# Kernel tuning notes

Measured on AMD Instinct MI355X. Metric: run time of the kernel, lower is better.

## Reference

```python
import jax, jax.numpy as jnp
import numpy as np

MAX_LENGTH = 10
SOS = 0
H = 1024
V = 32000
B = 256
S = 64


def setup_inputs() -> dict:
    key = jax.random.key(0)
    ks = jax.random.split(key, 16)
    sc = 1.0 / np.sqrt(H)
    return {
        "encoder_outputs": jax.random.normal(ks[0], (B, S, H), jnp.float32),
        "encoder_hidden": jax.random.normal(ks[1], (1, B, H), jnp.float32),
        "target_tensor": jax.random.randint(ks[2], (B, MAX_LENGTH), 0, V),
        "embedding": jax.random.normal(ks[3], (V, H), jnp.float32),
        "Wa_w": jax.random.uniform(ks[4], (H, H), jnp.float32, -sc, sc),
        "Wa_b": jax.random.uniform(ks[5], (H,), jnp.float32, -sc, sc),
        "Ua_w": jax.random.uniform(ks[6], (H, H), jnp.float32, -sc, sc),
        "Ua_b": jax.random.uniform(ks[7], (H,), jnp.float32, -sc, sc),
        "Va_w": jax.random.uniform(ks[8], (1, H), jnp.float32, -sc, sc),
        "Va_b": jax.random.uniform(ks[9], (1,), jnp.float32, -sc, sc),
        "gru_w_ih": jax.random.uniform(ks[10], (3 * H, 2 * H), jnp.float32, -sc, sc),
        "gru_w_hh": jax.random.uniform(ks[11], (3 * H, H), jnp.float32, -sc, sc),
        "gru_b_ih": jax.random.uniform(ks[12], (3 * H,), jnp.float32, -sc, sc),
        "gru_b_hh": jax.random.uniform(ks[13], (3 * H,), jnp.float32, -sc, sc),
        "out_w": jax.random.uniform(ks[14], (V, H), jnp.float32, -sc, sc),
        "out_b": jax.random.uniform(ks[15], (V,), jnp.float32, -sc, sc),
    }


def reference(encoder_outputs, encoder_hidden, target_tensor, embedding,
              Wa_w, Wa_b, Ua_w, Ua_b, Va_w, Va_b,
              gru_w_ih, gru_w_hh, gru_b_ih, gru_b_hh, out_w, out_b):
    keys = encoder_outputs                      # [B,S,H]
    # Ua(keys) is step-invariant: hoist out of the decode loop.
    Uk = jnp.einsum('bsh,kh->bsk', keys, Ua_w) + Ua_b  # [B,S,H]
    h0 = encoder_hidden[0]                      # [B,H]
    # teacher forcing: input at step i is SOS for i=0 else target[:, i-1]
    toks = jnp.concatenate(
        [jnp.full((B, 1), SOS, dtype=target_tensor.dtype),
         target_tensor[:, :MAX_LENGTH - 1]], axis=1).T  # [T,B]

    def step(h, tok):
        emb = embedding[tok]                               # [B,H] (dropout = identity in eval)
        wq = jnp.dot(h, Wa_w.T) + Wa_b                     # [B,H]
        e = jnp.tanh(wq[:, None, :] + Uk)                  # [B,S,H]
        scores = jnp.einsum('bsh,h->bs', e, Va_w[0]) + Va_b[0]
        w = jax.nn.softmax(scores, axis=-1)                # [B,S]
        ctx = jnp.einsum('bs,bsh->bh', w, keys)            # [B,H]
        x = jnp.concatenate([emb, ctx], axis=-1)           # [B,2H]
        gi = jnp.dot(x, gru_w_ih.T) + gru_b_ih             # [B,3H]
        gh = jnp.dot(h, gru_w_hh.T) + gru_b_hh             # [B,3H]
        ir, iz, inn = jnp.split(gi, 3, axis=-1)
        hr, hz, hn = jnp.split(gh, 3, axis=-1)
        r = jax.nn.sigmoid(ir + hr)
        z = jax.nn.sigmoid(iz + hz)
        n = jnp.tanh(inn + r * hn)
        h2 = (1.0 - z) * n + z * h                         # [B,H]
        logits = jnp.dot(h2, out_w.T) + out_b              # [B,V]
        return h2, (logits, w)

    h_last, (logits, attn) = jax.lax.scan(step, h0, toks)
    dec_out = jax.nn.log_softmax(jnp.transpose(logits, (1, 0, 2)), axis=-1)  # [B,T,V]
    attentions = jnp.transpose(attn, (1, 0, 2))            # [B,T,S]
    return dec_out, h_last[None, :, :], attentions
```

## Files before the change

kernel.cpp:

```cpp
#include <hip/hip_runtime.h>
#include <math.h>

#define H 1024
#define V 32000
#define B 256
#define S 64
#define T 10

#define GBK 32

typedef __attribute__((ext_vector_type(8))) short bf16x8;
typedef __attribute__((ext_vector_type(4))) float f32x4;

static __device__ __forceinline__ unsigned short f2bf(float f) {
  unsigned int u = __float_as_uint(f);
  u += 0x7fff + ((u >> 16) & 1);
  return (unsigned short)(u >> 16);
}
static __device__ __forceinline__ float bf2f(unsigned short u) {
  return __uint_as_float(((unsigned int)u) << 16);
}
static __device__ __forceinline__ float fast_tanh(float x) {
  float e = __expf(2.f * x);
  return 1.f - 2.f * __builtin_amdgcn_rcpf(e + 1.f);
}
static __device__ __forceinline__ float fast_sigmoid(float x) {
  return __builtin_amdgcn_rcpf(1.f + __expf(-x));
}

static __device__ __forceinline__ void load_lds16(const void* g, void* l) {
  __builtin_amdgcn_global_load_lds(
      (const __attribute__((address_space(1))) unsigned int*)g,
      (__attribute__((address_space(3))) unsigned int*)l, 16, 0, 0);
}

static __device__ __forceinline__ int lds_off(int row, int g) {
  return row * GBK + ((g ^ ((row >> 1) & 3)) * 8);
}

template <int TM, int TN, int MODE, int GRIDMODE, int STAGES>
__global__ __launch_bounds__(256) void gemm_mfma(
    const unsigned short* __restrict__ A, const unsigned short* __restrict__ W,
    const float* __restrict__ aux, float* __restrict__ C,
    int M, int N, int K, int ldc) {
  constexpr int FM = TM / 32;
  constexpr int FN = TN / 32;
  constexpr int CA = TM / 64;
  constexpr int CB = TN / 64;
  constexpr int LOADS = CA + CB;
  constexpr int F = (STAGES >= 3) ? (STAGES - 2) : 0;

  __shared__ unsigned short lsA[STAGES][TM * GBK];
  __shared__ unsigned short lsB[STAGES][TN * GBK];
  const int tid = threadIdx.x;
  const int lane = tid & 63;
  const int w = tid >> 6;

  int mIdx, nIdx;
  if constexpr (GRIDMODE == 1) {
    const int nwg = gridDim.x * gridDim.y;
    const int orig = blockIdx.y * gridDim.x + blockIdx.x;
    const int q = nwg >> 3, rr = nwg & 7;
    const int xcd = orig & 7, rest = orig >> 3;
    const int wgid =
        (xcd < rr ? xcd * (q + 1) : rr * (q + 1) + (xcd - rr) * q) + rest;
    mIdx = wgid % gridDim.x;
    nIdx = wgid / gridDim.x;
  } else {
    mIdx = blockIdx.y;
    nIdx = blockIdx.x;
  }
  const int mBase = mIdx * TM;
  const int nBase = nIdx * TN;
  const int rowBase = (w >> 1) * (TM / 2);
  const int colBase = (w & 1) * (TN / 2);

  const int fr = lane & 15;
  const int fkU = lane >> 4;
  const int fg = lane >> 4;

  f32x4 acc[FM][FN] = {};

  auto STAGE = [&](int buf, int k0) {
#pragma unroll
    for (int i = 0; i < CA; ++i) {
      int chunk = i * 256 + tid;
      int row = chunk >> 2;
      int u = chunk & 3;
      int col = (u ^ ((row >> 1) & 3)) * 8;
      load_lds16(A + (size_t)(mBase + row) * K + k0 + col,
                 &lsA[buf][chunk * 8]);
    }
#pragma unroll
    for (int i = 0; i < CB; ++i) {
      int chunk = i * 256 + tid;
      int row = chunk >> 2;
      int u = chunk & 3;
      int col = (u ^ ((row >> 1) & 3)) * 8;
      load_lds16(W + (size_t)(nBase + row) * K + k0 + col,
                 &lsB[buf][chunk * 8]);
    }
  };

  const int NT = K / GBK;
  for (int s = 0; s <= F && s < NT; ++s) STAGE(s % STAGES, s * GBK);

  for (int t = 0; t < NT; ++t) {
    const int rem = NT - 1 - t;
    if (rem >= F) {
      asm volatile("s_waitcnt vmcnt(%0)\n\ts_barrier" :: "i"(F * LOADS)
                   : "memory");
    } else if (rem == 2) {
      asm volatile("s_waitcnt vmcnt(%0)\n\ts_barrier" :: "i"(2 * LOADS)
                   : "memory");
    } else if (rem == 1) {
      asm volatile("s_waitcnt vmcnt(%0)\n\ts_barrier" :: "i"(1 * LOADS)
                   : "memory");
    } else {
      asm volatile("s_waitcnt vmcnt(0)\n\ts_barrier" ::: "memory");
    }
    if (t + F + 1 < NT) STAGE((t + F + 1) % STAGES, (t + F + 1) * GBK);

    const int cb = t % STAGES;
    bf16x8 af[FM], bfr[FN];
#pragma unroll
    for (int m = 0; m < FM; ++m)
      af[m] = *(const bf16x8*)&lsA[cb][lds_off(rowBase + m * 16 + fr, fkU)];
#pragma unroll
    for (int n = 0; n < FN; ++n)
      bfr[n] = *(const bf16x8*)&lsB[cb][lds_off(colBase + n * 16 + fr, fkU)];
#pragma unroll
    for (int m = 0; m < FM; ++m)
#pragma unroll
      for (int n = 0; n < FN; ++n)
        acc[m][n] = __builtin_amdgcn_mfma_f32_16x16x32_bf16(
            af[m], bfr[n], acc[m][n], 0, 0, 0);
  }

#pragma unroll
  for (int m = 0; m < FM; ++m) {
    int colg[FN];
    float bv[FN];
#pragma unroll
    for (int n = 0; n < FN; ++n) {
      colg[n] = nBase + colBase + n * 16 + fr;
      if constexpr (MODE != 2) bv[n] = aux[colg[n]];
    }
#pragma unroll
    for (int r = 0; r < 4; ++r) {
      const int rowg = mBase + rowBase + m * 16 + fg * 4 + r;
      float v[FN];
#pragma unroll
      for (int n = 0; n < FN; ++n) {
        if constexpr (MODE == 2)
          v[n] = acc[m][n][r] + aux[(size_t)rowg * ldc + colg[n]];
        else
          v[n] = acc[m][n][r] + bv[n];
        C[(size_t)rowg * ldc + colg[n]] = v[n];
      }
    }
  }
}

__global__ __launch_bounds__(256) void gemm_gru3(
    const unsigned short* __restrict__ A,
    const unsigned short* __restrict__ W3,
    const float* __restrict__ giE_t,
    const float* __restrict__ wqgh,
    const float* __restrict__ h_in,
    float* __restrict__ h_out,
    unsigned short* __restrict__ h_out_bf,
    unsigned char* __restrict__ h_out_f8) {
  constexpr int BK = 64;
  constexpr int STAGES = 3;
  constexpr int LOADS = 5;
  __shared__ unsigned short lsA[STAGES][64 * BK];
  __shared__ unsigned short lsW[STAGES][96 * BK];
  const int tid = threadIdx.x;
  const int lane = tid & 63;
  const int w = tid >> 6;
  const int mBase = blockIdx.x * 64;
  const int jBase = blockIdx.y * 32;
  const int fr = lane & 15;
  const int fkU = lane >> 4;
  const int fg = lane >> 4;

  f32x4 acc[6] = {};

  auto STAGE = [&](int buf, int k0) {
#pragma unroll
    for (int i = 0; i < 2; ++i) {
      int c = i * 256 + tid;
      int row = c >> 3, u = c & 7;
      int col = (u ^ (row & 7)) * 8;
      load_lds16(A + (size_t)(mBase + row) * H + k0 + col, &lsA[buf][c * 8]);
    }
#pragma unroll
    for (int i = 0; i < 3; ++i) {
      int c = i * 256 + tid;
      int wr = c >> 3, u = c & 7;
      int gate = wr >> 5, jj = wr & 31;
      int col = (u ^ (wr & 7)) * 8;
      load_lds16(W3 + (size_t)(gate * H + jBase + jj) * H + k0 + col,
                 &lsW[buf][c * 8]);
    }
  };

  const int NT = H / BK;
  STAGE(0, 0);
  STAGE(1, BK);
  for (int t = 0; t < NT; ++t) {
    const int rem = NT - 1 - t;
    if (rem >= 1) {
      asm volatile("s_waitcnt vmcnt(%0)\n\ts_barrier" :: "i"(LOADS)
                   : "memory");
    } else {
      asm volatile("s_waitcnt vmcnt(0)\n\ts_barrier" ::: "memory");
    }
    if (t + 2 < NT) STAGE((t + 2) % STAGES, (t + 2) * BK);
    const int cb = t % STAGES;
    const int arow = w * 16 + fr;
#pragma unroll
    for (int ks = 0; ks < 2; ++ks) {
      const int u = ks * 4 + fkU;
      bf16x8 af =
          *(const bf16x8*)&lsA[cb][arow * BK + ((u ^ (arow & 7)) * 8)];
#pragma unroll
      for (int n = 0; n < 6; ++n) {
        int wr = n * 16 + fr;
        bf16x8 bf =
            *(const bf16x8*)&lsW[cb][wr * BK + ((u ^ (wr & 7)) * 8)];
        acc[n] = __builtin_amdgcn_mfma_f32_16x16x32_bf16(af, bf, acc[n],
                                                         0, 0, 0);
      }
    }
  }

#pragma unroll
  for (int r = 0; r < 4; ++r) {
    const int b = mBase + w * 16 + fg * 4 + r;
    const float* giE_row = giE_t + (size_t)b * 3 * H;
    const float* gh_row = wqgh + (size_t)b * 4 * H + H;
#pragma unroll
    for (int jjg = 0; jjg < 2; ++jjg) {
      const int col = jBase + jjg * 16 + fr;
      float gr = acc[0 + jjg][r] + giE_row[col];
      float gz = acc[2 + jjg][r] + giE_row[H + col];
      float gn = acc[4 + jjg][r] + giE_row[2 * H + col];
      float rr = fast_sigmoid(gr + gh_row[col]);
      float zz = fast_sigmoid(gz + gh_row[H + col]);
      float nn = fast_tanh(gn + rr * gh_row[2 * H + col]);
      float hp = h_in[(size_t)b * H + col];
      float ho = (1.f - zz) * nn + zz * hp;
      h_out[(size_t)b * H + col] = ho;
      h_out_bf[(size_t)b * H + col] = f2bf(ho);
      int p8 = __builtin_amdgcn_cvt_pk_fp8_f32(ho, ho, 0, false);
      h_out_f8[(size_t)b * H + col] = (unsigned char)(p8 & 0xff);
    }
  }
}

template <int MODE>
__global__ __launch_bounds__(256) void gemm_fp8(
    const unsigned char* __restrict__ A8, const unsigned char* __restrict__ W8,
    const float* __restrict__ bias, unsigned short* __restrict__ Cb,
    unsigned char* __restrict__ C8, float* __restrict__ partials,
    int M, int N, int K, int ldc, int pstride) {
  constexpr int BK = 64;
  __shared__ __align__(16) unsigned char lsA[2][128 * BK];
  __shared__ __align__(16) unsigned char lsB[2][128 * BK];
  const int tid = threadIdx.x;
  const int lane = tid & 63;
  const int w = tid >> 6;

  const int nwg = gridDim.x * gridDim.y;
  const int orig = blockIdx.y * gridDim.x + blockIdx.x;
  const int q = nwg >> 3, rr = nwg & 7;
  const int xcd = orig & 7, rest = orig >> 3;
  const int wgid =
      (xcd < rr ? xcd * (q + 1) : rr * (q + 1) + (xcd - rr) * q) + rest;
  const int mIdx = wgid % gridDim.x;
  const int nIdx = wgid / gridDim.x;
  const int mBase = mIdx * 128;
  const int nBase = nIdx * 128;
  const int rowBase = (w >> 1) * 64;
  const int colBase = (w & 1) * 64;
  const int fr = lane & 15;
  const int fkU = lane >> 4;
  const int fg = lane >> 4;

  f32x4 acc[4][4] = {};

  auto STAGE = [&](int buf, int k0) {
#pragma unroll
    for (int i = 0; i < 2; ++i) {
      int c = i * 256 + tid;
      int row = c >> 2;
      int u = c & 3;
      int col = (u ^ ((row >> 1) & 3)) * 16;
      load_lds16(A8 + (size_t)(mBase + row) * K + k0 + col, &lsA[buf][c * 16]);
    }
#pragma unroll
    for (int i = 0; i < 2; ++i) {
      int c = i * 256 + tid;
      int row = c >> 2;
      int u = c & 3;
      int col = (u ^ ((row >> 1) & 3)) * 16;
      load_lds16(W8 + (size_t)(nBase + row) * K + k0 + col, &lsB[buf][c * 16]);
    }
  };

  const int NT = K / BK;
  STAGE(0, 0);
  int cb = 0;
  for (int t = 0; t < NT; ++t) {
    asm volatile("s_waitcnt vmcnt(0)\n\ts_barrier" ::: "memory");
    if (t + 1 < NT) STAGE(cb ^ 1, (t + 1) * BK);
#pragma unroll
    for (int ks = 0; ks < 2; ++ks) {
      const int u = ks * 2 + (fkU >> 1);
      const int sub = (fkU & 1) * 8;
      long long af[4], bf[4];
#pragma unroll
      for (int m = 0; m < 4; ++m) {
        int row = rowBase + m * 16 + fr;
        af[m] = *(const long long*)
            &lsA[cb][row * BK + ((u ^ ((row >> 1) & 3)) << 4) + sub];
      }
#pragma unroll
      for (int n = 0; n < 4; ++n) {
        int row = colBase + n * 16 + fr;
        bf[n] = *(const long long*)
            &lsB[cb][row * BK + ((u ^ ((row >> 1) & 3)) << 4) + sub];
      }
#pragma unroll
      for (int m = 0; m < 4; ++m)
#pragma unroll
        for (int n = 0; n < 4; ++n)
          acc[m][n] = __builtin_amdgcn_mfma_f32_16x16x32_fp8_fp8(
              af[m], bf[n], acc[m][n], 0, 0, 0);
    }
    cb ^= 1;
  }

#pragma unroll
  for (int m = 0; m < 4; ++m) {
    int colg[4];
    float bv[4];
#pragma unroll
    for (int n = 0; n < 4; ++n) {
      colg[n] = nBase + colBase + n * 16 + fr;
      bv[n] = bias[colg[n]];
    }
#pragma unroll
    for (int r = 0; r < 4; ++r) {
      const int rowg = mBase + rowBase + m * 16 + fg * 4 + r;
      float v[4];
#pragma unroll
      for (int n = 0; n < 4; ++n) {
        v[n] = acc[m][n][r] + bv[n];
        if constexpr (MODE == 3) {
          Cb[(size_t)rowg * ldc + colg[n]] = f2bf(v[n]);
        } else {
          int pk = __builtin_amdgcn_cvt_pk_fp8_f32(v[n], v[n], 0, false);
          C8[(size_t)rowg * ldc + colg[n]] = (unsigned char)(pk & 0xff);
        }
      }
      if constexpr (MODE == 3) {
        float mx = fmaxf(fmaxf(v[0], v[1]), fmaxf(v[2], v[3]));
        mx = fmaxf(mx, __shfl_xor(mx, 1, 64));
        mx = fmaxf(mx, __shfl_xor(mx, 2, 64));
        mx = fmaxf(mx, __shfl_xor(mx, 4, 64));
        mx = fmaxf(mx, __shfl_xor(mx, 8, 64));
        float se = __expf(v[0] - mx) + __expf(v[1] - mx) +
                   __expf(v[2] - mx) + __expf(v[3] - mx);
        se += __shfl_xor(se, 1, 64);
        se += __shfl_xor(se, 2, 64);
        se += __shfl_xor(se, 4, 64);
        se += __shfl_xor(se, 8, 64);
        if (fr == 0) {
          float2* pp = (float2*)partials;
          pp[(size_t)rowg * pstride + nIdx * 2 + (w & 1)] =
              make_float2(mx, se);
        }
      }
    }
  }
}

static __device__ __forceinline__ void cvt8(const float* src,
                                            unsigned short* dst, size_t i) {
  float4 a = *(const float4*)&src[i];
  float4 b = *(const float4*)&src[i + 4];
  ushort4 lo, hi;
  lo.x = f2bf(a.x); lo.y = f2bf(a.y); lo.z = f2bf(a.z); lo.w = f2bf(a.w);
  hi.x = f2bf(b.x); hi.y = f2bf(b.y); hi.z = f2bf(b.z); hi.w = f2bf(b.w);
  *(ushort4*)&dst[i] = lo;
  *(ushort4*)&dst[i + 4] = hi;
}

__global__ __launch_bounds__(256) void cvt_bf16_kernel(
    const float* __restrict__ src, unsigned short* __restrict__ dst) {
  cvt8(src, dst, ((size_t)blockIdx.x * 256 + threadIdx.x) * 8);
}

__global__ __launch_bounds__(256) void prep_weights(
    const float* __restrict__ Wa_w, const float* __restrict__ w_hh,
    const float* __restrict__ w_ih, unsigned short* __restrict__ fusedW,
    unsigned short* __restrict__ Wemb, unsigned short* __restrict__ Wctx) {
  const int blk = blockIdx.x;
  if (blk < 512) {
    cvt8(Wa_w, fusedW, ((size_t)blk * 256 + threadIdx.x) * 8);
  } else if (blk < 2048) {
    cvt8(w_hh, fusedW + (size_t)H * H,
         ((size_t)(blk - 512) * 256 + threadIdx.x) * 8);
  } else {
    size_t base = ((size_t)(blk - 2048) * 256 + threadIdx.x) * 8;
    int row = (int)(base >> 11);
    int col = (int)(base & 2047);
    float4 a = *(const float4*)&w_ih[base];
    float4 b = *(const float4*)&w_ih[base + 4];
    ushort4 lo, hi;
    lo.x = f2bf(a.x); lo.y = f2bf(a.y); lo.z = f2bf(a.z); lo.w = f2bf(a.w);
    hi.x = f2bf(b.x); hi.y = f2bf(b.y); hi.z = f2bf(b.z); hi.w = f2bf(b.w);
    unsigned short* dst = (col < H) ? (Wemb + (size_t)row * H + col)
                                    : (Wctx + (size_t)row * H + col - H);
    *(ushort4*)dst = lo;
    *(ushort4*)(dst + 4) = hi;
  }
}

__global__ __launch_bounds__(256) void cvt_fp8_kernel(
    const float* __restrict__ src, unsigned int* __restrict__ dst) {
  size_t i = (size_t)blockIdx.x * 256 + threadIdx.x;
  float4 a = ((const float4*)src)[i * 2];
  float4 b = ((const float4*)src)[i * 2 + 1];
  int lo = __builtin_amdgcn_cvt_pk_fp8_f32(a.x, a.y, 0, false);
  lo = __builtin_amdgcn_cvt_pk_fp8_f32(a.z, a.w, lo, true);
  int hi = __builtin_amdgcn_cvt_pk_fp8_f32(b.x, b.y, 0, false);
  hi = __builtin_amdgcn_cvt_pk_fp8_f32(b.z, b.w, hi, true);
  ((int2*)dst)[i] = make_int2(lo, hi);
}

__global__ __launch_bounds__(256) void build_fused_bias(
    const float* __restrict__ Wa_b, const float* __restrict__ b_hh,
    float* __restrict__ fb) {
  int i = blockIdx.x * 256 + threadIdx.x;
  fb[i] = (i < H) ? Wa_b[i] : b_hh[i - H];
}

__global__ __launch_bounds__(256) void embed_all_kernel(
    const int* __restrict__ target, const float* __restrict__ emb,
    unsigned short* __restrict__ embAll) {
  int idx = blockIdx.x * 256 + threadIdx.x;
  int h8 = (idx & 127) * 8;
  int tb = idx >> 7;
  int t = tb >> 8;
  int b = tb & 255;
  int tok = (t == 0) ? 0 : target[b * T + (t - 1)];
  const float* e = emb + (size_t)tok * H + h8;
  float4 a = *(const float4*)e;
  float4 c = *(const float4*)(e + 4);
  ushort4 lo, hi;
  lo.x = f2bf(a.x); lo.y = f2bf(a.y); lo.z = f2bf(a.z); lo.w = f2bf(a.w);
  hi.x = f2bf(c.x); hi.y = f2bf(c.y); hi.z = f2bf(c.z); hi.w = f2bf(c.w);
  unsigned short* d = embAll + (size_t)tb * H + h8;
  *(ushort4*)d = lo;
  *(ushort4*)(d + 4) = hi;
}

__global__ __launch_bounds__(256) void attn_fused_kernel(
    const float* __restrict__ wqgh, const unsigned char* __restrict__ Uk_f8,
    const unsigned char* __restrict__ keys_f8,
    const float* __restrict__ Va_w, const float* __restrict__ Va_b,
    float* __restrict__ out_attn, unsigned short* __restrict__ ctx_bf, int t) {
  const int b = blockIdx.x;
  const int tid = threadIdx.x;
  __shared__ float wqs[H];
  __shared__ float vas[H];
  __shared__ float sw[S];

  ((float4*)wqs)[tid] = ((const float4*)(wqgh + (size_t)b * 4 * H))[tid];
  ((float4*)vas)[tid] = ((const float4*)Va_w)[tid];
  __syncthreads();

  const int s = tid >> 2;
  const int hc = (tid & 3) * 256;
  const unsigned char* uk = Uk_f8 + ((size_t)b * S + s) * H + hc;
  float sum = 0.f;
#pragma unroll 4
  for (int i = 0; i < 256; i += 8) {
    uint2 u = *(const uint2*)&uk[i];
    float uv[8];
    uv[0] = __builtin_amdgcn_cvt_f32_fp8(u.x, 0);
    uv[1] = __builtin_amdgcn_cvt_f32_fp8(u.x, 1);
    uv[2] = __builtin_amdgcn_cvt_f32_fp8(u.x, 2);
    uv[3] = __builtin_amdgcn_cvt_f32_fp8(u.x, 3);
    uv[4] = __builtin_amdgcn_cvt_f32_fp8(u.y, 0);
    uv[5] = __builtin_amdgcn_cvt_f32_fp8(u.y, 1);
    uv[6] = __builtin_amdgcn_cvt_f32_fp8(u.y, 2);
    uv[7] = __builtin_amdgcn_cvt_f32_fp8(u.y, 3);
#pragma unroll
    for (int j = 0; j < 8; ++j) {
      float e = fast_tanh(wqs[hc + i + j] + uv[j]);
      sum += e * vas[hc + i + j];
    }
  }
  sum += __shfl_xor(sum, 1, 64);
  sum += __shfl_xor(sum, 2, 64);
  if ((tid & 3) == 0) sw[s] = sum + Va_b[0];
  __syncthreads();

  if (tid < 64) {
    float v = sw[tid];
    float m = v;
    for (int off = 32; off > 0; off >>= 1) m = fmaxf(m, __shfl_xor(m, off, 64));
    float e = __expf(v - m);
    float sm = e;
    for (int off = 32; off > 0; off >>= 1) sm += __shfl_xor(sm, off, 64);
    float wv = e / sm;
    sw[tid] = wv;
    out_attn[((size_t)b * T + t) * S + tid] = wv;
  }
  __syncthreads();

  const unsigned char* kb = keys_f8 + (size_t)b * S * H + tid * 4;
  float c0 = 0.f, c1 = 0.f, c2 = 0.f, c3 = 0.f;
#pragma unroll 8
  for (int s2 = 0; s2 < S; ++s2) {
    float wv = sw[s2];
    unsigned int kv = *(const unsigned int*)&kb[(size_t)s2 * H];
    c0 += wv * __builtin_amdgcn_cvt_f32_fp8(kv, 0);
    c1 += wv * __builtin_amdgcn_cvt_f32_fp8(kv, 1);
    c2 += wv * __builtin_amdgcn_cvt_f32_fp8(kv, 2);
    c3 += wv * __builtin_amdgcn_cvt_f32_fp8(kv, 3);
  }
  ushort4 o;
  o.x = f2bf(c0); o.y = f2bf(c1); o.z = f2bf(c2); o.w = f2bf(c3);
  *(ushort4*)&ctx_bf[(size_t)b * H + tid * 4] = o;
}

__global__ __launch_bounds__(256) void logsm_reduce_kernel(
    const float* __restrict__ partials, float* __restrict__ ls, int P) {
  const int row = blockIdx.x;
  const int tid = threadIdx.x;
  const float2* pp = (const float2*)partials + (size_t)row * P;
  __shared__ float red[256];
  float mx = -INFINITY;
  for (int i = tid; i < P; i += 256) mx = fmaxf(mx, pp[i].x);
  red[tid] = mx;
  __syncthreads();
  for (int off = 128; off > 0; off >>= 1) {
    if (tid < off) red[tid] = fmaxf(red[tid], red[tid + off]);
    __syncthreads();
  }
  mx = red[0];
  __syncthreads();
  float sm = 0.f;
  for (int i = tid; i < P; i += 256) sm += pp[i].y * __expf(pp[i].x - mx);
  red[tid] = sm;
  __syncthreads();
  for (int off = 128; off > 0; off >>= 1) {
    if (tid < off) red[tid] += red[tid + off];
    __syncthreads();
  }
  if (tid == 0) ls[row] = mx + __logf(red[0]);
}

__global__ __launch_bounds__(256) void logsm_sub_kernel(
    const unsigned short* __restrict__ logits_bf, const float* __restrict__ ls,
    float* __restrict__ dec) {
  const int tb = blockIdx.y;
  const int t = tb >> 8;
  const int b = tb & 255;
  const int i8 = (blockIdx.x * 256 + threadIdx.x) * 8;
  if (i8 < V) {
    float l = ls[tb];
    const unsigned short* src = logits_bf + (size_t)tb * V + i8;
    bf16x8 u = *(const bf16x8*)src;
    float* d = dec + (size_t)b * T * V + (size_t)t * V + i8;
    float4 o0, o1;
    o0.x = bf2f((unsigned short)u[0]) - l; o0.y = bf2f((unsigned short)u[1]) - l;
    o0.z = bf2f((unsigned short)u[2]) - l; o0.w = bf2f((unsigned short)u[3]) - l;
    o1.x = bf2f((unsigned short)u[4]) - l; o1.y = bf2f((unsigned short)u[5]) - l;
    o1.z = bf2f((unsigned short)u[6]) - l; o1.w = bf2f((unsigned short)u[7]) - l;
    *(float4*)d = o0;
    *(float4*)(d + 4) = o1;
  }
}

__global__ __launch_bounds__(256) void copy_kernel(
    const float* __restrict__ src, float* __restrict__ dst, int n) {
  int i = blockIdx.x * 256 + threadIdx.x;
  if (i < n) dst[i] = src[i];
}

extern "C" void kernel_launch(void* const* d_in, const int* in_sizes, int n_in,
                              void* d_out, int out_size, void* d_ws, size_t ws_size,
                              hipStream_t stream) {
  const float* keys       = (const float*)d_in[0];
  const float* enc_hidden = (const float*)d_in[1];
  const int*   target     = (const int*)d_in[2];
  const float* embedding  = (const float*)d_in[3];
  const float* Wa_w = (const float*)d_in[4];
  const float* Wa_b = (const float*)d_in[5];
  const float* Ua_w = (const float*)d_in[6];
  const float* Ua_b = (const float*)d_in[7];
  const float* Va_w = (const float*)d_in[8];
  const float* Va_b = (const float*)d_in[9];
  const float* gru_w_ih = (const float*)d_in[10];
  const float* gru_w_hh = (const float*)d_in[11];
  const float* gru_b_ih = (const float*)d_in[12];
  const float* gru_b_hh = (const float*)d_in[13];
  const float* out_w = (const float*)d_in[14];
  const float* out_b = (const float*)d_in[15];

  float* out = (float*)d_out;
  float* out_dec  = out;
  float* out_h    = out + (size_t)B * T * V;
  float* out_attn = out + (size_t)B * T * V + (size_t)B * H;

  char* p = (char*)d_ws;
  unsigned char*  keys_f8 = (unsigned char*)p;  p += (size_t)B * S * H;
  unsigned char*  outw8   = (unsigned char*)p;  p += (size_t)V * H;
  unsigned char*  Uaw8    = (unsigned char*)p;  p += (size_t)H * H;
  unsigned short* fusedW  = (unsigned short*)p; p += (size_t)4 * H * H * 2;
  float*          fusedB  = (float*)p;          p += (size_t)4 * H * 4;
  unsigned short* Wemb_bf = (unsigned short*)p; p += (size_t)3 * H * H * 2;
  unsigned short* Wctx_bf = (unsigned short*)p; p += (size_t)3 * H * H * 2;
  unsigned short* embAll  = (unsigned short*)p; p += (size_t)T * B * H * 2;
  unsigned char*  Uk_f8   = (unsigned char*)p;  p += (size_t)B * S * H;
  float*          giE     = (float*)p;          p += (size_t)T * B * 3 * H * 4;
  float*          wqgh    = (float*)p;          p += (size_t)B * 4 * H * 4;
  unsigned short* ctx_bf  = (unsigned short*)p; p += (size_t)B * H * 2;
  float*          hA      = (float*)p;          p += (size_t)B * H * 4;
  float*          hB      = (float*)p;          p += (size_t)B * H * 4;
  unsigned short* hAll    = (unsigned short*)p; p += (size_t)(T + 1) * B * H * 2;
  unsigned char*  hAll8   = (unsigned char*)p;  p += (size_t)T * B * H;
  unsigned short* logits_bf = (unsigned short*)p; p += (size_t)T * B * V * 2;
  float*          parts   = (float*)p;          p += (size_t)T * B * 500 * 2 * 4;
  float*          ls      = (float*)p;          p += (size_t)T * B * 4;

  cvt_fp8_kernel<<<(B * S * H) / 2048, 256, 0, stream>>>(
      keys, (unsigned int*)keys_f8);
  cvt_fp8_kernel<<<((size_t)V * H) / 2048, 256, 0, stream>>>(
      out_w, (unsigned int*)outw8);
  cvt_fp8_kernel<<<(H * H) / 2048, 256, 0, stream>>>(
      Ua_w, (unsigned int*)Uaw8);
  prep_weights<<<5120, 256, 0, stream>>>(Wa_w, gru_w_hh, gru_w_ih,
                                         fusedW, Wemb_bf, Wctx_bf);
  build_fused_bias<<<(4 * H) / 256, 256, 0, stream>>>(Wa_b, gru_b_hh, fusedB);
  embed_all_kernel<<<(T * B * H / 8) / 256, 256, 0, stream>>>(target, embedding,
                                                              embAll);
  cvt_bf16_kernel<<<(B * H) / 2048, 256, 0, stream>>>(enc_hidden, hAll);

  gemm_fp8<4><<<dim3((B * S) / 128, H / 128), 256, 0, stream>>>(
      keys_f8, Uaw8, Ua_b, nullptr, Uk_f8, nullptr, B * S, H, H, H, 0);
  gemm_mfma<128, 128, 0, 1, 2>
      <<<dim3((T * B) / 128, 3 * H / 128), 256, 0, stream>>>(
          embAll, Wemb_bf, gru_b_ih, giE, T * B, 3 * H, H, 3 * H);

  const float* h_in = enc_hidden;
  float* hbufs[2] = {hA, hB};

  for (int t = 0; t < T; ++t) {
    const unsigned short* hbf_in = hAll + (size_t)t * B * H;
    unsigned short* hbf_out = hAll + (size_t)(t + 1) * B * H;
    unsigned char* h8_out = hAll8 + (size_t)t * B * H;
    float* h_out = hbufs[t & 1];

    gemm_mfma<64, 64, 0, 1, 5><<<dim3(B / 64, 4 * H / 64), 256, 0, stream>>>(
        hbf_in, fusedW, fusedB, wqgh, B, 4 * H, H, 4 * H);
    attn_fused_kernel<<<B, 256, 0, stream>>>(
        wqgh, Uk_f8, keys_f8, Va_w, Va_b, out_attn, ctx_bf, t);
    gemm_gru3<<<dim3(B / 64, H / 32), 256, 0, stream>>>(
        ctx_bf, Wctx_bf, giE + (size_t)t * B * 3 * H, wqgh, h_in, h_out,
        hbf_out, h8_out);

    h_in = h_out;
  }

  gemm_fp8<3><<<dim3((T * B) / 128, V / 128), 256, 0, stream>>>(
      hAll8, outw8, out_b, logits_bf, nullptr, parts, T * B, V, H, V, 500);
  logsm_reduce_kernel<<<T * B, 256, 0, stream>>>(parts, ls, 500);
  logsm_sub_kernel<<<dim3((V + 2047) / 2048, T * B), 256, 0, stream>>>(
      logits_bf, ls, out_dec);

  copy_kernel<<<(B * H + 255) / 256, 256, 0, stream>>>(h_in, out_h, B * H);
}
```

Baseline: 895.4 us.

## Store fp8 hidden states in MFMA fragment layout and load A directly to registers

The GRU kernel now writes fp8 hidden states into a tiled layout where each 16-row by 8-column chunk is contiguous, matching the MFMA A-operand fragment. The vocab projection GEMM then loads A fragments straight from global memory into registers, skipping the LDS staging for A; only W goes through LDS, double-buffered with paired register sets. This cuts LDS traffic and shared-memory footprint for the large logits GEMM. In exchange, A fragments are reloaded per block from global/L2 with 8-byte accesses, and the GRU epilogue's fp8 stores become scattered.

```diff
diff --git a/kernel.cpp b/kernel.cpp
--- a/kernel.cpp
+++ b/kernel.cpp
@@ -36,6 +36,11 @@
 
 static __device__ __forceinline__ int lds_off(int row, int g) {
   return row * GBK + ((g ^ ((row >> 1) & 3)) * 8);
+}
+
+static __device__ __forceinline__ size_t a8i_off(int row, int k) {
+  return ((size_t)(row >> 4) * 128 + (k >> 3)) * 128 + (row & 15) * 8 +
+         (k & 7);
 }
 
 template <int TM, int TN, int MODE, int GRIDMODE, int STAGES>
@@ -170,7 +175,8 @@
     const float* __restrict__ h_in,
     float* __restrict__ h_out,
     unsigned short* __restrict__ h_out_bf,
-    unsigned char* __restrict__ h_out_f8) {
+    unsigned char* __restrict__ hAll8i,
+    int t) {
   constexpr int BK = 64;
   constexpr int STAGES = 3;
   constexpr int LOADS = 5;
@@ -209,16 +215,16 @@
   const int NT = H / BK;
   STAGE(0, 0);
   STAGE(1, BK);
-  for (int t = 0; t < NT; ++t) {
-    const int rem = NT - 1 - t;
+  for (int tt = 0; tt < NT; ++tt) {
+    const int rem = NT - 1 - tt;
     if (rem >= 1) {
       asm volatile("s_waitcnt vmcnt(%0)\n\ts_barrier" :: "i"(LOADS)
                    : "memory");
     } else {
       asm volatile("s_waitcnt vmcnt(0)\n\ts_barrier" ::: "memory");
     }
-    if (t + 2 < NT) STAGE((t + 2) % STAGES, (t + 2) * BK);
-    const int cb = t % STAGES;
+    if (tt + 2 < NT) STAGE((tt + 2) % STAGES, (tt + 2) * BK);
+    const int cb = tt % STAGES;
     const int arow = w * 16 + fr;
 #pragma unroll
     for (int ks = 0; ks < 2; ++ks) {
@@ -239,6 +245,7 @@
 #pragma unroll
   for (int r = 0; r < 4; ++r) {
     const int b = mBase + w * 16 + fg * 4 + r;
+    const int tb = t * B + b;
     const float* giE_row = giE_t + (size_t)b * 3 * H;
     const float* gh_row = wqgh + (size_t)b * 4 * H + H;
 #pragma unroll
@@ -255,17 +262,15 @@
       h_out[(size_t)b * H + col] = ho;
       h_out_bf[(size_t)b * H + col] = f2bf(ho);
       int p8 = __builtin_amdgcn_cvt_pk_fp8_f32(ho, ho, 0, false);
-      h_out_f8[(size_t)b * H + col] = (unsigned char)(p8 & 0xff);
-    }
-  }
-}
-
-template <int MODE>
-__global__ __launch_bounds__(256) void gemm_fp8(
+      hAll8i[a8i_off(tb, col)] = (unsigned char)(p8 & 0xff);
+    }
+  }
+}
+
+__global__ __launch_bounds__(256) void gemm_fp8_uk(
     const unsigned char* __restrict__ A8, const unsigned char* __restrict__ W8,
-    const float* __restrict__ bias, unsigned short* __restrict__ Cb,
-    unsigned char* __restrict__ C8, float* __restrict__ partials,
-    int M, int N, int K, int ldc, int pstride) {
+    const float* __restrict__ bias, unsigned char* __restrict__ C8,
+    int M, int N, int K, int ldc) {
   constexpr int BK = 64;
   __shared__ __align__(16) unsigned char lsA[2][128 * BK];
   __shared__ __align__(16) unsigned char lsB[2][128 * BK];
@@ -345,6 +350,136 @@
 
 #pragma unroll
   for (int m = 0; m < 4; ++m) {
+#pragma unroll
+    for (int r = 0; r < 4; ++r) {
+      const int rowg = mBase + rowBase + m * 16 + fg * 4 + r;
+#pragma unroll
+      for (int n = 0; n < 4; ++n) {
+        const int colg = nBase + colBase + n * 16 + fr;
+        float v = acc[m][n][r] + bias[colg];
+        int pk = __builtin_amdgcn_cvt_pk_fp8_f32(v, v, 0, false);
+        C8[(size_t)rowg * ldc + colg] = (unsigned char)(pk & 0xff);
+      }
+    }
+  }
+}
+
+__global__ __launch_bounds__(256) void gemm_fp8_vocab(
+    const unsigned char* __restrict__ A8i, const unsigned char* __restrict__ W8,
+    const float* __restrict__ bias, unsigned short* __restrict__ Cb,
+    float* __restrict__ partials, int M, int N, int K, int ldc, int pstride) {
+  constexpr int BK = 64;
+  __shared__ __align__(16) unsigned char lsB[2][128 * BK];
+  const int tid = threadIdx.x;
+  const int lane = tid & 63;
+  const int w = tid >> 6;
+
+  const int nwg = gridDim.x * gridDim.y;
+  const int orig = blockIdx.y * gridDim.x + blockIdx.x;
+  const int q = nwg >> 3, rr = nwg & 7;
+  const int xcd = orig & 7, rest = orig >> 3;
+  const int wgid =
+      (xcd < rr ? xcd * (q + 1) : rr * (q + 1) + (xcd - rr) * q) + rest;
+  const int mIdx = wgid % gridDim.x;
+  const int nIdx = wgid / gridDim.x;
+  const int mBase = mIdx * 128;
+  const int nBase = nIdx * 128;
+  const int rowBase = (w >> 1) * 64;
+  const int colBase = (w & 1) * 64;
+  const int fr = lane & 15;
+  const int fkU = lane >> 4;
+  const int fg = lane >> 4;
+  const int mtile = (mBase + rowBase) >> 4;
+
+  f32x4 acc[4][4] = {};
+
+  auto STAGE_W = [&](int buf, int k0) {
+#pragma unroll
+    for (int i = 0; i < 2; ++i) {
+      int c = i * 256 + tid;
+      int row = c >> 2;
+      int u = c & 3;
+      int col = (u ^ ((row >> 1) & 3)) * 16;
+      load_lds16(W8 + (size_t)(nBase + row) * K + k0 + col, &lsB[buf][c * 16]);
+    }
+  };
+
+  long long afA[2][4], afB[2][4];
+  auto LOADA_A = [&](int k0) {
+#pragma unroll
+    for (int ks = 0; ks < 2; ++ks) {
+      const int kk = (k0 >> 3) + ks * 4 + fkU;
+#pragma unroll
+      for (int m = 0; m < 4; ++m)
+        afA[ks][m] = *(const long long*)
+            &A8i[((size_t)(mtile + m) * 128 + kk) * 128 + fr * 8];
+    }
+  };
+  auto LOADA_B = [&](int k0) {
+#pragma unroll
+    for (int ks = 0; ks < 2; ++ks) {
+      const int kk = (k0 >> 3) + ks * 4 + fkU;
+#pragma unroll
+      for (int m = 0; m < 4; ++m)
+        afB[ks][m] = *(const long long*)
+            &A8i[((size_t)(mtile + m) * 128 + kk) * 128 + fr * 8];
+    }
+  };
+
+  const int NT = K / BK;
+  LOADA_A(0);
+  STAGE_W(0, 0);
+  for (int t = 0; t < NT; t += 2) {
+    asm volatile("s_waitcnt vmcnt(0)\n\ts_barrier" ::: "memory");
+    if (t + 1 < NT) {
+      STAGE_W(1, (t + 1) * BK);
+      LOADA_B((t + 1) * BK);
+    }
+#pragma unroll
+    for (int ks = 0; ks < 2; ++ks) {
+      const int u = ks * 2 + (fkU >> 1);
+      const int sub = (fkU & 1) * 8;
+      long long bf[4];
+#pragma unroll
+      for (int n = 0; n < 4; ++n) {
+        int row = colBase + n * 16 + fr;
+        bf[n] = *(const long long*)
+            &lsB[0][row * BK + ((u ^ ((row >> 1) & 3)) << 4) + sub];
+      }
+#pragma unroll
+      for (int m = 0; m < 4; ++m)
+#pragma unroll
+        for (int n = 0; n < 4; ++n)
+          acc[m][n] = __builtin_amdgcn_mfma_f32_16x16x32_fp8_fp8(
+              afA[ks][m], bf[n], acc[m][n], 0, 0, 0);
+    }
+    asm volatile("s_waitcnt vmcnt(0)\n\ts_barrier" ::: "memory");
+    if (t + 2 < NT) {
+      STAGE_W(0, (t + 2) * BK);
+      LOADA_A((t + 2) * BK);
+    }
+#pragma unroll
+    for (int ks = 0; ks < 2; ++ks) {
+      const int u = ks * 2 + (fkU >> 1);
+      const int sub = (fkU & 1) * 8;
+      long long bf[4];
+#pragma unroll
+      for (int n = 0; n < 4; ++n) {
+        int row = colBase + n * 16 + fr;
+        bf[n] = *(const long long*)
+            &lsB[1][row * BK + ((u ^ ((row >> 1) & 3)) << 4) + sub];
+      }
+#pragma unroll
+      for (int m = 0; m < 4; ++m)
+#pragma unroll
+        for (int n = 0; n < 4; ++n)
+          acc[m][n] = __builtin_amdgcn_mfma_f32_16x16x32_fp8_fp8(
+              afB[ks][m], bf[n], acc[m][n], 0, 0, 0);
+    }
+  }
+
+#pragma unroll
+  for (int m = 0; m < 4; ++m) {
     int colg[4];
     float bv[4];
 #pragma unroll
@@ -359,30 +494,22 @@
 #pragma unroll
       for (int n = 0; n < 4; ++n) {
         v[n] = acc[m][n][r] + bv[n];
-        if constexpr (MODE == 3) {
-          Cb[(size_t)rowg * ldc + colg[n]] = f2bf(v[n]);
-        } else {
-          int pk = __builtin_amdgcn_cvt_pk_fp8_f32(v[n], v[n], 0, false);
-          C8[(size_t)rowg * ldc + colg[n]] = (unsigned char)(pk & 0xff);
-        }
+        Cb[(size_t)rowg * ldc + colg[n]] = f2bf(v[n]);
       }
-      if constexpr (MODE == 3) {
-        float mx = fmaxf(fmaxf(v[0], v[1]), fmaxf(v[2], v[3]));
-        mx = fmaxf(mx, __shfl_xor(mx, 1, 64));
-        mx = fmaxf(mx, __shfl_xor(mx, 2, 64));
-        mx = fmaxf(mx, __shfl_xor(mx, 4, 64));
-        mx = fmaxf(mx, __shfl_xor(mx, 8, 64));
-        float se = __expf(v[0] - mx) + __expf(v[1] - mx) +
-                   __expf(v[2] - mx) + __expf(v[3] - mx);
-        se += __shfl_xor(se, 1, 64);
-        se += __shfl_xor(se, 2, 64);
-        se += __shfl_xor(se, 4, 64);
-        se += __shfl_xor(se, 8, 64);
-        if (fr == 0) {
-          float2* pp = (float2*)partials;
-          pp[(size_t)rowg * pstride + nIdx * 2 + (w & 1)] =
-              make_float2(mx, se);
-        }
+      float mx = fmaxf(fmaxf(v[0], v[1]), fmaxf(v[2], v[3]));
+      mx = fmaxf(mx, __shfl_xor(mx, 1, 64));
+      mx = fmaxf(mx, __shfl_xor(mx, 2, 64));
+      mx = fmaxf(mx, __shfl_xor(mx, 4, 64));
+      mx = fmaxf(mx, __shfl_xor(mx, 8, 64));
+      float se = __expf(v[0] - mx) + __expf(v[1] - mx) +
+                 __expf(v[2] - mx) + __expf(v[3] - mx);
+      se += __shfl_xor(se, 1, 64);
+      se += __shfl_xor(se, 2, 64);
+      se += __shfl_xor(se, 4, 64);
+      se += __shfl_xor(se, 8, 64);
+      if (fr == 0) {
+        float2* pp = (float2*)partials;
+        pp[(size_t)rowg * pstride + nIdx * 2 + (w & 1)] = make_float2(mx, se);
       }
     }
   }
@@ -636,7 +763,7 @@
   float*          hA      = (float*)p;          p += (size_t)B * H * 4;
   float*          hB      = (float*)p;          p += (size_t)B * H * 4;
   unsigned short* hAll    = (unsigned short*)p; p += (size_t)(T + 1) * B * H * 2;
-  unsigned char*  hAll8   = (unsigned char*)p;  p += (size_t)T * B * H;
+  unsigned char*  hAll8i  = (unsigned char*)p;  p += (size_t)T * B * H;
   unsigned short* logits_bf = (unsigned short*)p; p += (size_t)T * B * V * 2;
   float*          parts   = (float*)p;          p += (size_t)T * B * 500 * 2 * 4;
   float*          ls      = (float*)p;          p += (size_t)T * B * 4;
@@ -654,8 +781,8 @@
                                                               embAll);
   cvt_bf16_kernel<<<(B * H) / 2048, 256, 0, stream>>>(enc_hidden, hAll);
 
-  gemm_fp8<4><<<dim3((B * S) / 128, H / 128), 256, 0, stream>>>(
-      keys_f8, Uaw8, Ua_b, nullptr, Uk_f8, nullptr, B * S, H, H, H, 0);
+  gemm_fp8_uk<<<dim3((B * S) / 128, H / 128), 256, 0, stream>>>(
+      keys_f8, Uaw8, Ua_b, Uk_f8, B * S, H, H, H);
   gemm_mfma<128, 128, 0, 1, 2>
       <<<dim3((T * B) / 128, 3 * H / 128), 256, 0, stream>>>(
           embAll, Wemb_bf, gru_b_ih, giE, T * B, 3 * H, H, 3 * H);
@@ -666,7 +793,6 @@
   for (int t = 0; t < T; ++t) {
     const unsigned short* hbf_in = hAll + (size_t)t * B * H;
     unsigned short* hbf_out = hAll + (size_t)(t + 1) * B * H;
-    unsigned char* h8_out = hAll8 + (size_t)t * B * H;
     float* h_out = hbufs[t & 1];
 
     gemm_mfma<64, 64, 0, 1, 5><<<dim3(B / 64, 4 * H / 64), 256, 0, stream>>>(
@@ -675,13 +801,13 @@
         wqgh, Uk_f8, keys_f8, Va_w, Va_b, out_attn, ctx_bf, t);
     gemm_gru3<<<dim3(B / 64, H / 32), 256, 0, stream>>>(
         ctx_bf, Wctx_bf, giE + (size_t)t * B * 3 * H, wqgh, h_in, h_out,
-        hbf_out, h8_out);
+        hbf_out, hAll8i, t);
 
     h_in = h_out;
   }
 
-  gemm_fp8<3><<<dim3((T * B) / 128, V / 128), 256, 0, stream>>>(
-      hAll8, outw8, out_b, logits_bf, nullptr, parts, T * B, V, H, V, 500);
+  gemm_fp8_vocab<<<dim3((T * B) / 128, V / 128), 256, 0, stream>>>(
+      hAll8i, outw8, out_b, logits_bf, parts, T * B, V, H, V, 500);
   logsm_reduce_kernel<<<T * B, 256, 0, stream>>>(parts, ls, 500);
   logsm_sub_kernel<<<dim3((V + 2047) / 2048, T * B), 256, 0, stream>>>(
       logits_bf, ls, out_dec);
```

New measurement: 892.1 us. Within noise of the previous version (-0.4%).
